# Kernel tuning notes

Hardware: AMD Instinct MI355X
Metric: run time of the kernel (lower is better)

## Reference

```python
import jax, jax.numpy as jnp
import numpy as np

B, T, C, H = 4, 2048, 1024, 16
HD = C // H  # head dim = 64


def _rope(x, pos):
    """Rotary embedding. x: [B,H,T,hd], pos: [B,T] int positions."""
    half = x.shape[-1] // 2
    inv_freq = 1.0 / (10000.0 ** (jnp.arange(half, dtype=jnp.float32) / half))
    ang = pos.astype(jnp.float32)[:, None, :, None] * inv_freq  # [B,1,T,half]
    cos, sin = jnp.cos(ang), jnp.sin(ang)
    x1, x2 = x[..., :half], x[..., half:]
    return jnp.concatenate([x1 * cos - x2 * sin, x1 * sin + x2 * cos], axis=-1)


def setup_inputs() -> dict:
    key = jax.random.key(0)
    k1, k2, k3 = jax.random.split(key, 3)
    x = jax.random.normal(k1, (B, T, C), dtype=jnp.float32)
    W_attn = jax.random.normal(k2, (C, 3 * C), dtype=jnp.float32) * (1.0 / np.sqrt(C))
    W_proj = jax.random.normal(k3, (C, C), dtype=jnp.float32) * (1.0 / np.sqrt(C))
    indices = jnp.broadcast_to(jnp.arange(T, dtype=jnp.int32)[None, :], (B, T))
    return {"x": x, "W_attn": W_attn, "W_proj": W_proj, "indices": indices}


def reference(x, W_attn, W_proj, indices):
    # QKV projection (bias=False)
    qkv = x @ W_attn  # [B,T,3C]
    q, k, v = jnp.split(qkv, 3, axis=-1)

    def to_heads(t):
        return t.reshape(B, T, H, HD).transpose(0, 2, 1, 3)  # [B,H,T,hd]

    q, k, v = to_heads(q), to_heads(k), to_heads(v)
    # RoPE on q and k at positions given by indices (pos_emb_closure.adapt_*)
    q = _rope(q, indices)
    k = _rope(k, indices)

    # attn_mask = k_indices <= q_indices, shape [B,1,T,T]
    mask = indices[:, None, None, :] <= indices[:, None, :, None]

    att = jnp.einsum("bhqd,bhkd->bhqk", q, k) * (1.0 / np.sqrt(HD))
    att = jnp.where(mask, att, jnp.float32(-jnp.inf))
    att = jax.nn.softmax(att, axis=-1)
    y = jnp.einsum("bhqk,bhkd->bhqd", att, v)  # [B,H,T,hd]
    y = y.transpose(0, 2, 1, 3).reshape(B, T, C)
    return y @ W_proj
```

## Files before the change

kernel.cpp:

```cpp
#include <hip/hip_runtime.h>
#include <math.h>

namespace {
constexpr int Bsz = 4;
constexpr int T   = 2048;
constexpr int C   = 1024;
constexpr int H   = 16;
constexpr int HD  = 64;

typedef short bf16x8 __attribute__((ext_vector_type(8)));
typedef float f32x4  __attribute__((ext_vector_type(4)));

#if defined(__has_builtin)
#if __has_builtin(__builtin_amdgcn_global_load_lds)
#define HAVE_GLL 1
typedef __attribute__((address_space(3))) unsigned int lds_u32_t;
typedef __attribute__((address_space(1))) unsigned int g_u32_t;
#define GLL16(gp, lp)                                                        \
  __builtin_amdgcn_global_load_lds((const g_u32_t*)(gp), (lds_u32_t*)(lp),   \
                                   16, 0, 0)
#endif
#endif

__device__ __forceinline__ unsigned short f2bf(float f) {
  unsigned int u = __builtin_bit_cast(unsigned int, f);
  u += 0x7FFFu + ((u >> 16) & 1u);
  return (unsigned short)(u >> 16);
}
__device__ __forceinline__ unsigned int pack_bf(float a, float b) {
  unsigned int ua = __builtin_bit_cast(unsigned int, a) + 0x8000u;
  unsigned int ub = __builtin_bit_cast(unsigned int, b) + 0x8000u;
  return __builtin_amdgcn_perm(ub, ua, 0x07060302u);
}
__device__ __forceinline__ float bf2f(unsigned short s) {
  unsigned int u = ((unsigned int)s) << 16;
  return __builtin_bit_cast(float, u);
}

__global__ __launch_bounds__(256) void f32_to_bf16_kernel(
    const float* __restrict__ in, unsigned short* __restrict__ out, int n4) {
  int i = blockIdx.x * 256 + threadIdx.x;
  if (i < n4) {
    float4 v = ((const float4*)in)[i];
    ushort4 o;
    o.x = f2bf(v.x); o.y = f2bf(v.y); o.z = f2bf(v.z); o.w = f2bf(v.w);
    ((ushort4*)out)[i] = o;
  }
}

__global__ __launch_bounds__(256) void transpose_bf16_kernel(
    const float* __restrict__ W, unsigned short* __restrict__ Wt, int K, int N) {
  __shared__ float tile[32][33];
  const int n0 = blockIdx.x * 32, k0 = blockIdx.y * 32;
  const int r = threadIdx.x >> 3, c4 = threadIdx.x & 7;
  float4 v = *(const float4*)(W + (size_t)(k0 + r) * N + n0 + c4 * 4);
  tile[r][c4 * 4 + 0] = v.x;
  tile[r][c4 * 4 + 1] = v.y;
  tile[r][c4 * 4 + 2] = v.z;
  tile[r][c4 * 4 + 3] = v.w;
  __syncthreads();
  ushort4 o;
  o.x = f2bf(tile[c4 * 4 + 0][r]);
  o.y = f2bf(tile[c4 * 4 + 1][r]);
  o.z = f2bf(tile[c4 * 4 + 2][r]);
  o.w = f2bf(tile[c4 * 4 + 3][r]);
  *(ushort4*)(Wt + (size_t)(n0 + r) * K + k0 + c4 * 4) = o;
}

template <int MODE>
__global__ __launch_bounds__(256) void gemm_bt(
    const unsigned short* __restrict__ A, const unsigned short* __restrict__ Bt,
    float* __restrict__ Cout, unsigned short* __restrict__ qp,
    unsigned short* __restrict__ kp, unsigned short* __restrict__ vp,
    int M, int N, int K) {
  __shared__ __align__(16) unsigned short As[128 * 32];
  __shared__ __align__(16) unsigned short Bs[128 * 32];
  const int tid = threadIdx.x;
  const int lane = tid & 63, w = tid >> 6;
  const int wr = w & 1, wc = w >> 1;
  const int l15 = lane & 15, quad = lane >> 4;
  const int m0 = blockIdx.y * 128, n0 = blockIdx.x * 128;

  const int srow = lane >> 2;
  const int schunk = (lane & 3) * 8;
  const unsigned short* gA = A + (size_t)(m0 + w * 32 + srow) * K + schunk;
  const unsigned short* gB = Bt + (size_t)(n0 + w * 32 + srow) * K + schunk;
  unsigned short* lA0 = &As[(w * 32) * 32 + lane * 8];
  unsigned short* lA1 = &As[(w * 32 + 16) * 32 + lane * 8];
  unsigned short* lB0 = &Bs[(w * 32) * 32 + lane * 8];
  unsigned short* lB1 = &Bs[(w * 32 + 16) * 32 + lane * 8];

  f32x4 acc[4][4] = {};

  for (int k0 = 0; k0 < K; k0 += 32) {
    __syncthreads();
#ifdef HAVE_GLL
    GLL16(gA + k0, lA0);
    GLL16(gA + (size_t)16 * K + k0, lA1);
    GLL16(gB + k0, lB0);
    GLL16(gB + (size_t)16 * K + k0, lB1);
#else
    *(uint4*)lA0 = *(const uint4*)(gA + k0);
    *(uint4*)lA1 = *(const uint4*)(gA + (size_t)16 * K + k0);
    *(uint4*)lB0 = *(const uint4*)(gB + k0);
    *(uint4*)lB1 = *(const uint4*)(gB + (size_t)16 * K + k0);
#endif
    __syncthreads();

    bf16x8 af[4], bfr[4];
#pragma unroll
    for (int mf = 0; mf < 4; ++mf)
      af[mf] = *(const bf16x8*)&As[(wr * 64 + mf * 16 + l15) * 32 + quad * 8];
#pragma unroll
    for (int nf = 0; nf < 4; ++nf)
      bfr[nf] = *(const bf16x8*)&Bs[(wc * 64 + nf * 16 + l15) * 32 + quad * 8];
#pragma unroll
    for (int mf = 0; mf < 4; ++mf)
#pragma unroll
      for (int nf = 0; nf < 4; ++nf)
        acc[mf][nf] = __builtin_amdgcn_mfma_f32_16x16x32_bf16(
            af[mf], bfr[nf], acc[mf][nf], 0, 0, 0);
  }

#pragma unroll
  for (int mf = 0; mf < 4; ++mf) {
    const int row0 = m0 + wr * 64 + mf * 16 + quad * 4;
#pragma unroll
    for (int nf = 0; nf < 4; ++nf) {
      if (MODE == 0) {
#pragma unroll
        for (int r = 0; r < 4; ++r) {
          const int col = n0 + wc * 64 + nf * 16 + l15;
          Cout[(size_t)(row0 + r) * N + col] = acc[mf][nf][r];
        }
      } else {
        const int col = n0 + wc * 64 + nf * 16 + l15;
        const int which = col >> 10;
        const int rem = col & (C - 1);
        const int h = rem >> 6, hd = rem & 63;
        const int b = row0 >> 11, t0 = row0 & (T - 1);
        if (which == 2) {
          ushort4 pv;
          pv.x = f2bf(acc[mf][nf][0]);
          pv.y = f2bf(acc[mf][nf][1]);
          pv.z = f2bf(acc[mf][nf][2]);
          pv.w = f2bf(acc[mf][nf][3]);
          *(ushort4*)(vp + (((size_t)(b * H + h)) * HD + hd) * T + t0) = pv;
        } else {
          unsigned short* dst = which == 0 ? qp : kp;
#pragma unroll
          for (int r = 0; r < 4; ++r)
            dst[(((size_t)(b * H + h)) * T + t0 + r) * HD + hd] =
                f2bf(acc[mf][nf][r]);
        }
      }
    }
  }
}

__global__ __launch_bounds__(256) void rope_bf16(unsigned short* __restrict__ q,
                                                 unsigned short* __restrict__ k,
                                                 const int* __restrict__ idx) {
  const size_t g = (size_t)blockIdx.x * 8 + (threadIdx.x >> 5);
  const int lane = threadIdx.x & 31;
  const int t = (int)(g & (size_t)(T - 1));
  const int bh = (int)(g >> 11);
  const int b = bh >> 4;
  const int pos = idx[b * T + t];
  const float inv = 1.0f / powf(10000.0f, (float)lane * (1.0f / 32.0f));
  float sn, cs;
  sincosf((float)pos * inv, &sn, &cs);
  const size_t base = g * (size_t)HD;
  float x1 = bf2f(q[base + lane]), x2 = bf2f(q[base + 32 + lane]);
  q[base + lane]      = f2bf(x1 * cs - x2 * sn);
  q[base + 32 + lane] = f2bf(x1 * sn + x2 * cs);
  x1 = bf2f(k[base + lane]);
  x2 = bf2f(k[base + 32 + lane]);
  k[base + lane]      = f2bf(x1 * cs - x2 * sn);
  k[base + 32 + lane] = f2bf(x1 * sn + x2 * cs);
}

__global__ __launch_bounds__(256) void flash_attn_mfma(
    const unsigned short* __restrict__ q, const unsigned short* __restrict__ k,
    const unsigned short* __restrict__ vt, const int* __restrict__ idx,
    unsigned short* __restrict__ y) {
  __shared__ __align__(16) unsigned short Ks[2][64][72];
  __shared__ __align__(16) unsigned short Vts[2][64][72];
  __shared__ __align__(16) unsigned short Pq[64][72];

  const int tid = threadIdx.x;
  const int lane = tid & 63, w = tid >> 6;
  const int l15 = lane & 15, quad = lane >> 4;
  const int bx = blockIdx.x, h = blockIdx.y, b = blockIdx.z;
  const size_t bh = (size_t)(b * H + h);
  const unsigned short* qg = q + bh * T * HD;
  const unsigned short* kg = k + bh * T * HD;
  const unsigned short* vg = vt + bh * HD * T;
  const int* idxb = idx + b * T;
  const float SC = 0.18033688f;

  const int r1 = tid >> 3, c1 = tid & 7;
  const int r2 = r1 + 32;

  for (int ti = 0; ti < 2; ++ti) {
    const int qt = (ti == 0) ? bx : 31 - bx;
    const int q0 = qt * 64;
    const int qrow = q0 + w * 16 + l15;

    const bf16x8 bq0 = *(const bf16x8*)(qg + (size_t)qrow * HD + quad * 8);
    const bf16x8 bq1 = *(const bf16x8*)(qg + (size_t)qrow * HD + 32 + quad * 8);
    const int pq = idxb[qrow];

    float m_run = -1e38f, l_run = 0.0f;
    f32x4 Oa[4] = {};

    {
      uint4 ka = *(const uint4*)(kg + (size_t)r1 * HD + c1 * 8);
      uint4 kb = *(const uint4*)(kg + (size_t)r2 * HD + c1 * 8);
      uint4 va = *(const uint4*)(vg + (size_t)r1 * T + c1 * 8);
      uint4 vb = *(const uint4*)(vg + (size_t)r2 * T + c1 * 8);
      __syncthreads();
      *(uint4*)&Ks[0][r1][c1 * 8] = ka;
      *(uint4*)&Ks[0][r2][c1 * 8] = kb;
      *(uint4*)&Vts[0][r1][c1 * 8] = va;
      *(uint4*)&Vts[0][r2][c1 * 8] = vb;
    }

    for (int kt = 0; kt <= qt; ++kt) {
      const int cur = kt & 1;
      const int k0 = kt * 64;
      __syncthreads();

      uint4 nka, nkb, nva, nvb;
      if (kt < qt) {
        const int kn = k0 + 64;
        nka = *(const uint4*)(kg + (size_t)(kn + r1) * HD + c1 * 8);
        nkb = *(const uint4*)(kg + (size_t)(kn + r2) * HD + c1 * 8);
        nva = *(const uint4*)(vg + (size_t)r1 * T + kn + c1 * 8);
        nvb = *(const uint4*)(vg + (size_t)r2 * T + kn + c1 * 8);
      }

      f32x4 Sa[4];
#pragma unroll
      for (int nf = 0; nf < 4; ++nf) {
        bf16x8 ak0 = *(const bf16x8*)&Ks[cur][nf * 16 + l15][quad * 8];
        bf16x8 ak1 = *(const bf16x8*)&Ks[cur][nf * 16 + l15][32 + quad * 8];
        f32x4 s = {};
        s = __builtin_amdgcn_mfma_f32_16x16x32_bf16(ak0, bq0, s, 0, 0, 0);
        s = __builtin_amdgcn_mfma_f32_16x16x32_bf16(ak1, bq1, s, 0, 0, 0);
        Sa[nf] = s;
      }

      float z[4][4];
#pragma unroll
      for (int nf = 0; nf < 4; ++nf) {
        const int4 pk4 = *(const int4*)(idxb + k0 + nf * 16 + quad * 4);
        z[nf][0] = (pk4.x > pq) ? -3e38f : Sa[nf][0] * SC;
        z[nf][1] = (pk4.y > pq) ? -3e38f : Sa[nf][1] * SC;
        z[nf][2] = (pk4.z > pq) ? -3e38f : Sa[nf][2] * SC;
        z[nf][3] = (pk4.w > pq) ? -3e38f : Sa[nf][3] * SC;
      }

      float mx = z[0][0];
#pragma unroll
      for (int nf = 0; nf < 4; ++nf)
#pragma unroll
        for (int r = 0; r < 4; ++r) mx = fmaxf(mx, z[nf][r]);
      mx = fmaxf(mx, __shfl_xor(mx, 16));
      mx = fmaxf(mx, __shfl_xor(mx, 32));
      const float mn = fmaxf(m_run, mx);
      const float alpha = exp2f(m_run - mn);
      m_run = mn;
      float sum = 0.0f;
#pragma unroll
      for (int nf = 0; nf < 4; ++nf)
#pragma unroll
        for (int r = 0; r < 4; ++r) {
          float p = exp2f(z[nf][r] - mn);
          z[nf][r] = p;
          sum += p;
        }
      sum += __shfl_xor(sum, 16);
      sum += __shfl_xor(sum, 32);
      l_run = l_run * alpha + sum;

#pragma unroll
      for (int nf = 0; nf < 4; ++nf) {
        uint2 pw;
        pw.x = pack_bf(z[nf][0], z[nf][1]);
        pw.y = pack_bf(z[nf][2], z[nf][3]);
        *(uint2*)&Pq[w * 16 + l15][nf * 16 + quad * 4] = pw;
      }

#pragma unroll
      for (int nfd = 0; nfd < 4; ++nfd)
#pragma unroll
        for (int r = 0; r < 4; ++r) Oa[nfd][r] *= alpha;

      asm volatile("s_waitcnt lgkmcnt(0)" ::: "memory");

      const bf16x8 bp0 = *(const bf16x8*)&Pq[w * 16 + l15][quad * 8];
      const bf16x8 bp1 = *(const bf16x8*)&Pq[w * 16 + l15][32 + quad * 8];

#pragma unroll
      for (int nfd = 0; nfd < 4; ++nfd) {
        bf16x8 av0 = *(const bf16x8*)&Vts[cur][nfd * 16 + l15][quad * 8];
        bf16x8 av1 = *(const bf16x8*)&Vts[cur][nfd * 16 + l15][32 + quad * 8];
        Oa[nfd] = __builtin_amdgcn_mfma_f32_16x16x32_bf16(av0, bp0, Oa[nfd], 0, 0, 0);
        Oa[nfd] = __builtin_amdgcn_mfma_f32_16x16x32_bf16(av1, bp1, Oa[nfd], 0, 0, 0);
      }

      if (kt < qt) {
        const int nxt = cur ^ 1;
        *(uint4*)&Ks[nxt][r1][c1 * 8] = nka;
        *(uint4*)&Ks[nxt][r2][c1 * 8] = nkb;
        *(uint4*)&Vts[nxt][r1][c1 * 8] = nva;
        *(uint4*)&Vts[nxt][r2][c1 * 8] = nvb;
      }
    }

    const float rl = 1.0f / l_run;
    const size_t base = ((size_t)b * T + qrow) * (size_t)C + h * HD;
#pragma unroll
    for (int nfd = 0; nfd < 4; ++nfd) {
      ushort4 o;
      o.x = f2bf(Oa[nfd][0] * rl);
      o.y = f2bf(Oa[nfd][1] * rl);
      o.z = f2bf(Oa[nfd][2] * rl);
      o.w = f2bf(Oa[nfd][3] * rl);
      *(ushort4*)(y + base + nfd * 16 + quad * 4) = o;
    }
  }
}

}

extern "C" void kernel_launch(void* const* d_in, const int* in_sizes, int n_in,
                              void* d_out, int out_size, void* d_ws,
                              size_t ws_size, hipStream_t stream) {
  const float* x      = (const float*)d_in[0];
  const float* W_attn = (const float*)d_in[1];
  const float* W_proj = (const float*)d_in[2];
  const int* indices  = (const int*)d_in[3];
  float* out = (float*)d_out;

  const size_t nM = (size_t)Bsz * T * C;
  unsigned short* xb  = (unsigned short*)d_ws;
  unsigned short* wat = xb + nM;
  unsigned short* wpt = wat + (size_t)3 * C * C;
  unsigned short* qp  = wpt + (size_t)C * C;
  unsigned short* kp  = qp + nM;
  unsigned short* vp  = kp + nM;
  unsigned short* yb  = vp + nM;

  f32_to_bf16_kernel<<<(int)(nM / 4 / 256), 256, 0, stream>>>(x, xb, (int)(nM / 4));
  transpose_bf16_kernel<<<dim3(3 * C / 32, C / 32), 256, 0, stream>>>(W_attn, wat, C, 3 * C);
  transpose_bf16_kernel<<<dim3(C / 32, C / 32), 256, 0, stream>>>(W_proj, wpt, C, C);
  gemm_bt<1><<<dim3(3 * C / 128, Bsz * T / 128), 256, 0, stream>>>(
      xb, wat, nullptr, qp, kp, vp, Bsz * T, 3 * C, C);
  rope_bf16<<<(Bsz * H * T) / 8, 256, 0, stream>>>(qp, kp, indices);
  flash_attn_mfma<<<dim3(16, H, Bsz), 256, 0, stream>>>(qp, kp, vp, indices, yb);
  gemm_bt<0><<<dim3(C / 128, Bsz * T / 128), 256, 0, stream>>>(
      yb, wpt, out, nullptr, nullptr, nullptr, Bsz * T, C, C);
}
```

Baseline: 346.1 us.

## Skip masking on unmasked tiles, lazy rescale, fold scale into RoPE, remap blocks

Folds the softmax scale into the RoPE of q so the attention kernel no longer multiplies scores. Precomputes per-key-tile maximum positions so the causal mask is applied only to tiles that can contain masked entries. Adds a lazy online-softmax rescale that skips updating the running max and rescaling O unless the max grows by more than a threshold. Also switches to the hardware bf16 pack instruction and remaps block indices for better spreading across CUs. The lazy rescale and the tile-level mask skip add numeric and index-order assumptions, and the 8.0 threshold in the exp2 domain could in principle cause overflow risk in accumulators.

```diff
diff --git a/kernel.cpp b/kernel.cpp
--- a/kernel.cpp
+++ b/kernel.cpp
@@ -27,14 +27,14 @@
   u += 0x7FFFu + ((u >> 16) & 1u);
   return (unsigned short)(u >> 16);
 }
-__device__ __forceinline__ unsigned int pack_bf(float a, float b) {
-  unsigned int ua = __builtin_bit_cast(unsigned int, a) + 0x8000u;
-  unsigned int ub = __builtin_bit_cast(unsigned int, b) + 0x8000u;
-  return __builtin_amdgcn_perm(ub, ua, 0x07060302u);
-}
 __device__ __forceinline__ float bf2f(unsigned short s) {
   unsigned int u = ((unsigned int)s) << 16;
   return __builtin_bit_cast(float, u);
+}
+__device__ __forceinline__ unsigned int cvtpk_bf16(float a, float b) {
+  unsigned int r;
+  asm("v_cvt_pk_bf16_f32 %0, %1, %2" : "=v"(r) : "v"(a), "v"(b));
+  return r;
 }
 
 __global__ __launch_bounds__(256) void f32_to_bf16_kernel(
@@ -170,10 +170,12 @@
   const float inv = 1.0f / powf(10000.0f, (float)lane * (1.0f / 32.0f));
   float sn, cs;
   sincosf((float)pos * inv, &sn, &cs);
+  const float SC = 0.18033688f;
+  const float snq = sn * SC, csq = cs * SC;
   const size_t base = g * (size_t)HD;
   float x1 = bf2f(q[base + lane]), x2 = bf2f(q[base + 32 + lane]);
-  q[base + lane]      = f2bf(x1 * cs - x2 * sn);
-  q[base + 32 + lane] = f2bf(x1 * sn + x2 * cs);
+  q[base + lane]      = f2bf(x1 * csq - x2 * snq);
+  q[base + 32 + lane] = f2bf(x1 * snq + x2 * csq);
   x1 = bf2f(k[base + lane]);
   x2 = bf2f(k[base + 32 + lane]);
   k[base + lane]      = f2bf(x1 * cs - x2 * sn);
@@ -187,17 +189,34 @@
   __shared__ __align__(16) unsigned short Ks[2][64][72];
   __shared__ __align__(16) unsigned short Vts[2][64][72];
   __shared__ __align__(16) unsigned short Pq[64][72];
+  __shared__ int kmaxs[32];
 
   const int tid = threadIdx.x;
   const int lane = tid & 63, w = tid >> 6;
   const int l15 = lane & 15, quad = lane >> 4;
-  const int bx = blockIdx.x, h = blockIdx.y, b = blockIdx.z;
-  const size_t bh = (size_t)(b * H + h);
+
+  const int flat = (blockIdx.z * H + blockIdx.y) * 16 + blockIdx.x;
+  const int slot = flat >> 3;
+  const int bh_i = (flat & 7) * 8 + (slot >> 4);
+  const int bx = slot & 15;
+  const int h = bh_i & (H - 1), b = bh_i >> 4;
+
+  const size_t bh = (size_t)bh_i;
   const unsigned short* qg = q + bh * T * HD;
   const unsigned short* kg = k + bh * T * HD;
   const unsigned short* vg = vt + bh * HD * T;
   const int* idxb = idx + b * T;
-  const float SC = 0.18033688f;
+
+  if (tid < 32) {
+    const int4* p4 = (const int4*)(idxb + (tid << 6));
+    int m = p4[0].x;
+#pragma unroll
+    for (int j = 0; j < 16; ++j) {
+      int4 v = p4[j];
+      m = max(m, max(max(v.x, v.y), max(v.z, v.w)));
+    }
+    kmaxs[tid] = m;
+  }
 
   const int r1 = tid >> 3, c1 = tid & 7;
   const int r2 = r1 + 32;
@@ -210,6 +229,11 @@
     const bf16x8 bq0 = *(const bf16x8*)(qg + (size_t)qrow * HD + quad * 8);
     const bf16x8 bq1 = *(const bf16x8*)(qg + (size_t)qrow * HD + 32 + quad * 8);
     const int pq = idxb[qrow];
+    int mq = pq;
+    mq = min(mq, __shfl_xor(mq, 1));
+    mq = min(mq, __shfl_xor(mq, 2));
+    mq = min(mq, __shfl_xor(mq, 4));
+    mq = min(mq, __shfl_xor(mq, 8));
 
     float m_run = -1e38f, l_run = 0.0f;
     f32x4 Oa[4] = {};
@@ -251,51 +275,58 @@
         Sa[nf] = s;
       }
 
-      float z[4][4];
-#pragma unroll
-      for (int nf = 0; nf < 4; ++nf) {
-        const int4 pk4 = *(const int4*)(idxb + k0 + nf * 16 + quad * 4);
-        z[nf][0] = (pk4.x > pq) ? -3e38f : Sa[nf][0] * SC;
-        z[nf][1] = (pk4.y > pq) ? -3e38f : Sa[nf][1] * SC;
-        z[nf][2] = (pk4.z > pq) ? -3e38f : Sa[nf][2] * SC;
-        z[nf][3] = (pk4.w > pq) ? -3e38f : Sa[nf][3] * SC;
-      }
-
-      float mx = z[0][0];
-#pragma unroll
-      for (int nf = 0; nf < 4; ++nf)
-#pragma unroll
-        for (int r = 0; r < 4; ++r) mx = fmaxf(mx, z[nf][r]);
+      if (kmaxs[kt] > mq) {
+#pragma unroll
+        for (int nf = 0; nf < 4; ++nf) {
+          const int4 pk4 = *(const int4*)(idxb + k0 + nf * 16 + quad * 4);
+          if (pk4.x > pq) Sa[nf][0] = -3e38f;
+          if (pk4.y > pq) Sa[nf][1] = -3e38f;
+          if (pk4.z > pq) Sa[nf][2] = -3e38f;
+          if (pk4.w > pq) Sa[nf][3] = -3e38f;
+        }
+      }
+
+      float m0 = fmaxf(fmaxf(Sa[0][0], Sa[0][1]), fmaxf(Sa[0][2], Sa[0][3]));
+      float m1 = fmaxf(fmaxf(Sa[1][0], Sa[1][1]), fmaxf(Sa[1][2], Sa[1][3]));
+      float m2 = fmaxf(fmaxf(Sa[2][0], Sa[2][1]), fmaxf(Sa[2][2], Sa[2][3]));
+      float m3 = fmaxf(fmaxf(Sa[3][0], Sa[3][1]), fmaxf(Sa[3][2], Sa[3][3]));
+      float mx = fmaxf(fmaxf(m0, m1), fmaxf(m2, m3));
       mx = fmaxf(mx, __shfl_xor(mx, 16));
       mx = fmaxf(mx, __shfl_xor(mx, 32));
-      const float mn = fmaxf(m_run, mx);
-      const float alpha = exp2f(m_run - mn);
-      m_run = mn;
-      float sum = 0.0f;
-#pragma unroll
-      for (int nf = 0; nf < 4; ++nf)
-#pragma unroll
-        for (int r = 0; r < 4; ++r) {
-          float p = exp2f(z[nf][r] - mn);
-          z[nf][r] = p;
-          sum += p;
-        }
+
+      if (!__all(mx <= m_run + 8.0f)) {
+        const float mn = fmaxf(m_run, mx);
+        const float alpha = exp2f(m_run - mn);
+        m_run = mn;
+        l_run *= alpha;
+#pragma unroll
+        for (int nfd = 0; nfd < 4; ++nfd)
+#pragma unroll
+          for (int r = 0; r < 4; ++r) Oa[nfd][r] *= alpha;
+      }
+
+      float s0 = 0.f, s1 = 0.f, s2 = 0.f, s3 = 0.f;
+#pragma unroll
+      for (int nf = 0; nf < 4; ++nf) {
+        float p0 = exp2f(Sa[nf][0] - m_run);
+        float p1 = exp2f(Sa[nf][1] - m_run);
+        float p2 = exp2f(Sa[nf][2] - m_run);
+        float p3 = exp2f(Sa[nf][3] - m_run);
+        Sa[nf][0] = p0; Sa[nf][1] = p1; Sa[nf][2] = p2; Sa[nf][3] = p3;
+        s0 += p0; s1 += p1; s2 += p2; s3 += p3;
+      }
+      float sum = (s0 + s1) + (s2 + s3);
       sum += __shfl_xor(sum, 16);
       sum += __shfl_xor(sum, 32);
-      l_run = l_run * alpha + sum;
+      l_run += sum;
 
 #pragma unroll
       for (int nf = 0; nf < 4; ++nf) {
         uint2 pw;
-        pw.x = pack_bf(z[nf][0], z[nf][1]);
-        pw.y = pack_bf(z[nf][2], z[nf][3]);
+        pw.x = cvtpk_bf16(Sa[nf][0], Sa[nf][1]);
+        pw.y = cvtpk_bf16(Sa[nf][2], Sa[nf][3]);
         *(uint2*)&Pq[w * 16 + l15][nf * 16 + quad * 4] = pw;
       }
-
-#pragma unroll
-      for (int nfd = 0; nfd < 4; ++nfd)
-#pragma unroll
-        for (int r = 0; r < 4; ++r) Oa[nfd][r] *= alpha;
 
       asm volatile("s_waitcnt lgkmcnt(0)" ::: "memory");
 
```

After: 327.2 us. 5.4% less time.
